# Kernel optimization log

Hardware: AMD Instinct MI355X
Metric: run time of the kernel (lower is better)

Reference implementation:

```python
import jax, jax.numpy as jnp
import numpy as np

EMBED_DIM = 1024
BATCH = 4
SEQ = 2048


def setup_inputs() -> dict:
    key = jax.random.key(0)
    ks = jax.random.split(key, 9)
    E = EMBED_DIM
    s = 1.0 / np.sqrt(E)
    inp = {
        "x": jax.random.normal(ks[0], (BATCH, SEQ, E), dtype=jnp.float32),
        "Wq": jax.random.uniform(ks[1], (E, E), jnp.float32, -s, s),
        "bq": jax.random.uniform(ks[2], (E,), jnp.float32, -s, s),
        "Wk": jax.random.uniform(ks[3], (E, E), jnp.float32, -s, s),
        "bk": jax.random.uniform(ks[4], (E,), jnp.float32, -s, s),
        "Wv": jax.random.uniform(ks[5], (E, E), jnp.float32, -s, s),
        "bv": jax.random.uniform(ks[6], (E,), jnp.float32, -s, s),
        "Wo": jax.random.uniform(ks[7], (E, E), jnp.float32, -s, s),
        "bo": jax.random.uniform(ks[8], (E,), jnp.float32, -s, s),
    }
    return inp


def reference(x, Wq, bq, Wk, bk, Wv, bv, Wo, bo):
    # x: [B, S, E]. Single-head attention over full embed_dim.
    scale = x.shape[-1] ** -0.5
    q = jnp.einsum("bse,ef->bsf", x, Wq.T) + bq
    k = jnp.einsum("bse,ef->bsf", x, Wk.T) + bk
    v = jnp.einsum("bse,ef->bsf", x, Wv.T) + bv
    scores = jnp.einsum("bqe,bke->bqk", q, k) * scale  # [B, S, S]
    attn = jax.nn.softmax(scores, axis=-1)             # dropout p=0 -> identity
    out = jnp.einsum("bqk,bke->bqe", attn, v)
    return jnp.einsum("bse,ef->bsf", out, Wo.T) + bo
```

## Files before the change

kernel.cpp:

```cpp
#include <hip/hip_runtime.h>
#include <hip/hip_bf16.h>


typedef __bf16 bf16_t;
typedef __bf16 bf16x8 __attribute__((ext_vector_type(8)));
typedef __bf16 bf16x4 __attribute__((ext_vector_type(4)));
typedef float  f32x16 __attribute__((ext_vector_type(16)));

__device__ __forceinline__ void async_copy16(const void* g, void* l) {
  __builtin_amdgcn_global_load_lds(
      (const __attribute__((address_space(1))) void*)g,
      (__attribute__((address_space(3))) void*)l, 16, 0, 0);
}

__device__ __forceinline__ void store_out(float* p, float v)  { *p = v; }
__device__ __forceinline__ void store_out(bf16_t* p, float v) { *p = (bf16_t)v; }

#define BM 128
#define BN 128
#define BKT 64

template <typename OutT, int NBIAS>
__global__ __launch_bounds__(256) void gemm_bt(
    const bf16_t* __restrict__ A, const bf16_t* __restrict__ B,
    OutT* __restrict__ C,
    const float* __restrict__ b0, const float* __restrict__ b1,
    const float* __restrict__ b2,
    int M, int N, int K, int lda, int ldb, int ldc, float scale,
    long long strideA, long long strideB, long long strideC) {
  const int z = blockIdx.z;
  A += (long long)z * strideA;
  B += (long long)z * strideB;
  C += (long long)z * strideC;

  int bx = blockIdx.x, by = blockIdx.y;
  {
    const int GX  = gridDim.x;
    const int id  = by * GX + bx;
    const int per = GX * 8;
    const int grp = id / per;
    const int rem = id - grp * per;
    by = grp * 8 + (rem & 7);
    bx = rem >> 3;
  }

  __shared__ __align__(16) bf16_t As[BM * BKT];
  __shared__ __align__(16) bf16_t Bs[BN * BKT];

  const int t    = threadIdx.x;
  const int lane = t & 63;
  const int w    = t >> 6;
  const int wm   = w & 1;
  const int wn   = w >> 1;
  const int tileM = by * BM;
  const int tileN = bx * BN;

  f32x16 acc[2][2] = {};

  for (int k0 = 0; k0 < K; k0 += BKT) {
#pragma unroll
    for (int i = 0; i < 4; ++i) {
      const int c   = t + 256 * i;
      const int row = c >> 3;
      const int cc  = c & 7;
      const int gcc = cc ^ (row & 7);
      const int ldsbase = ((t & ~63) + 256 * i) * 8;
      async_copy16(A + (long long)(tileM + row) * lda + k0 + gcc * 8, &As[ldsbase]);
      async_copy16(B + (long long)(tileN + row) * ldb + k0 + gcc * 8, &Bs[ldsbase]);
    }
    __syncthreads();

#pragma unroll
    for (int s = 0; s < 4; ++s) {
      const int kc = s + 4 * (lane >> 5);
      bf16x8 af[2], bfr[2];
#pragma unroll
      for (int ti = 0; ti < 2; ++ti) {
        const int row = wm * 64 + ti * 32 + (lane & 31);
        af[ti] = *(const bf16x8*)&As[row * BKT + ((kc ^ (row & 7)) * 8)];
      }
#pragma unroll
      for (int tj = 0; tj < 2; ++tj) {
        const int row = wn * 64 + tj * 32 + (lane & 31);
        bfr[tj] = *(const bf16x8*)&Bs[row * BKT + ((kc ^ (row & 7)) * 8)];
      }
#pragma unroll
      for (int ti = 0; ti < 2; ++ti)
#pragma unroll
        for (int tj = 0; tj < 2; ++tj)
          acc[ti][tj] = __builtin_amdgcn_mfma_f32_32x32x16_bf16(
              af[ti], bfr[tj], acc[ti][tj], 0, 0, 0);
    }
    __syncthreads();
  }

#pragma unroll
  for (int tj = 0; tj < 2; ++tj) {
    const int col = tileN + wn * 64 + tj * 32 + (lane & 31);
    float bv = 0.f;
    if (NBIAS == 1) bv = b0[col];
    if (NBIAS == 3) {
      const float* bp = col < 1024 ? b0 : (col < 2048 ? b1 : b2);
      bv = bp[col & 1023];
    }
#pragma unroll
    for (int ti = 0; ti < 2; ++ti) {
      const int rowb = tileM + wm * 64 + ti * 32 + 4 * (lane >> 5);
#pragma unroll
      for (int r = 0; r < 16; ++r) {
        const int row = rowb + (r & 3) + 8 * (r >> 2);
        store_out(&C[(long long)row * ldc + col], acc[ti][tj][r] * scale + bv);
      }
    }
  }
}

__global__ __launch_bounds__(256) void cast_all(
    const float4* __restrict__ w0, const float4* __restrict__ w1,
    const float4* __restrict__ w2, const float4* __restrict__ w3,
    const float4* __restrict__ x,
    bf16x4* __restrict__ wdst, bf16x4* __restrict__ xdst) {
  const int N4W = 1 << 18;
  const int id = blockIdx.x * 256 + threadIdx.x;
  const float4* src;
  bf16x4* dst;
  if (id < 4 * N4W) {
    const int z = id >> 18;
    src = (z == 0 ? w0 : z == 1 ? w1 : z == 2 ? w2 : w3) + (id & (N4W - 1));
    dst = wdst + id;
  } else {
    const int i = id - 4 * N4W;
    src = x + i;
    dst = xdst + i;
  }
  const float4 v = *src;
  bf16x4 o;
  o[0] = (bf16_t)v.x; o[1] = (bf16_t)v.y; o[2] = (bf16_t)v.z; o[3] = (bf16_t)v.w;
  *dst = o;
}

__global__ __launch_bounds__(256) void transpose_bf16(
    const bf16_t* __restrict__ in, bf16_t* __restrict__ out, int R, int C,
    int ldin, long long sIn, long long sOut) {
  in  += (long long)blockIdx.z * sIn;
  out += (long long)blockIdx.z * sOut;
  __shared__ bf16_t tile[32][33];
  const int tx = threadIdx.x, ty = threadIdx.y;
  const int x = blockIdx.x * 32 + tx;
  const int y0 = blockIdx.y * 32;
#pragma unroll
  for (int j = 0; j < 32; j += 8)
    tile[ty + j][tx] = in[(long long)(y0 + ty + j) * ldin + x];
  __syncthreads();
  const int x2 = y0 + tx;
  const int y2 = blockIdx.x * 32;
#pragma unroll
  for (int j = 0; j < 32; j += 8)
    out[(long long)(y2 + ty + j) * R + x2] = tile[tx][ty + j];
}

__global__ __launch_bounds__(256) void softmax_rows(
    const bf16_t* __restrict__ S, bf16_t* __restrict__ P, int cols) {
  const long long row = blockIdx.x;
  const bf16x8* inp = (const bf16x8*)(S + row * cols);
  bf16x8* outp      = (bf16x8*)(P + row * cols);
  const int t = threadIdx.x;
  const int w = t >> 6, lane = t & 63;

  const bf16x8 v = inp[t];
  float f[8];
#pragma unroll
  for (int j = 0; j < 8; ++j) f[j] = (float)v[j];

  float m = f[0];
#pragma unroll
  for (int j = 1; j < 8; ++j) m = fmaxf(m, f[j]);
#pragma unroll
  for (int off = 32; off > 0; off >>= 1) m = fmaxf(m, __shfl_xor(m, off));

  __shared__ float red[8];
  if (lane == 0) red[w] = m;
  __syncthreads();
  m = fmaxf(fmaxf(red[0], red[1]), fmaxf(red[2], red[3]));

  float e[8], sum = 0.f;
#pragma unroll
  for (int j = 0; j < 8; ++j) { e[j] = __expf(f[j] - m); sum += e[j]; }
#pragma unroll
  for (int off = 32; off > 0; off >>= 1) sum += __shfl_xor(sum, off);
  if (lane == 0) red[4 + w] = sum;
  __syncthreads();
  sum = red[4] + red[5] + red[6] + red[7];

  const float inv = 1.f / sum;
  bf16x8 o;
#pragma unroll
  for (int j = 0; j < 8; ++j) o[j] = (bf16_t)(e[j] * inv);
  outp[t] = o;
}

extern "C" void kernel_launch(void* const* d_in, const int* in_sizes, int n_in,
                              void* d_out, int out_size, void* d_ws, size_t ws_size,
                              hipStream_t stream) {
  const int E = 1024, S = 2048, B = 4;
  const int BS = B * S;

  const float* x  = (const float*)d_in[0];
  const float* Wq = (const float*)d_in[1];
  const float* bq = (const float*)d_in[2];
  const float* Wk = (const float*)d_in[3];
  const float* bk = (const float*)d_in[4];
  const float* Wv = (const float*)d_in[5];
  const float* bv = (const float*)d_in[6];
  const float* Wo = (const float*)d_in[7];
  const float* bo = (const float*)d_in[8];
  float* out = (float*)d_out;

  char* w = (char*)d_ws;
  const size_t MB = 1ull << 20;
  bf16_t* Wqkvb = (bf16_t*)(w + 0 * MB);
  bf16_t* Wob   = Wqkvb + 3 * E * E;
  bf16_t* xb    = (bf16_t*)(w + 8 * MB);
  bf16_t* QKVb  = (bf16_t*)(w + 24 * MB);
  bf16_t* VTb   = (bf16_t*)(w + 72 * MB);
  bf16_t* Sb    = (bf16_t*)(w + 88 * MB);
  bf16_t* Pb    = (bf16_t*)(w + 8 * MB);
  bf16_t* Ob    = (bf16_t*)(w + 40 * MB);

  {
    const int totalBlocks = ((4 << 18) + (1 << 21)) / 256;
    cast_all<<<totalBlocks, 256, 0, stream>>>(
        (const float4*)Wq, (const float4*)Wk, (const float4*)Wv,
        (const float4*)Wo, (const float4*)x, (bf16x4*)Wqkvb, (bf16x4*)xb);
  }

  gemm_bt<bf16_t, 3><<<dim3(3 * E / BN, BS / BM, 1), 256, 0, stream>>>(
      xb, Wqkvb, QKVb, bq, bk, bv,
      BS, 3 * E, E, E, E, 3 * E, 1.f, 0, 0, 0);

  transpose_bf16<<<dim3(E / 32, S / 32, B), dim3(32, 8), 0, stream>>>(
      QKVb + 2 * E, VTb, S, E, 3 * E, (long long)S * 3 * E, (long long)E * S);

  gemm_bt<bf16_t, 0><<<dim3(S / BN, S / BM, B), 256, 0, stream>>>(
      QKVb, QKVb + E, Sb, nullptr, nullptr, nullptr,
      S, S, E, 3 * E, 3 * E, S, 0.03125f,
      (long long)S * 3 * E, (long long)S * 3 * E, (long long)S * S);

  softmax_rows<<<BS, 256, 0, stream>>>(Sb, Pb, S);

  gemm_bt<bf16_t, 0><<<dim3(E / BN, S / BM, B), 256, 0, stream>>>(
      Pb, VTb, Ob, nullptr, nullptr, nullptr,
      S, E, S, S, S, E, 1.f,
      (long long)S * S, (long long)E * S, (long long)S * E);

  gemm_bt<float, 1><<<dim3(E / BN, BS / BM, 1), 256, 0, stream>>>(
      Ob, Wob, out, bo, nullptr, nullptr,
      BS, E, E, E, E, E, 1.f, 0, 0, 0);
}
```

Baseline: 292.2 us.

## Fuse softmax into score and PV GEMM epilogues, compute V transposed directly

```diff
diff --git a/kernel.cpp b/kernel.cpp
--- a/kernel.cpp
+++ b/kernel.cpp
@@ -20,18 +20,19 @@
 #define BN 128
 #define BKT 64
 
-template <typename OutT, int NBIAS>
+template <typename OutT, int BIAS, int EPI>
 __global__ __launch_bounds__(256) void gemm_bt(
     const bf16_t* __restrict__ A, const bf16_t* __restrict__ B,
     OutT* __restrict__ C,
     const float* __restrict__ b0, const float* __restrict__ b1,
-    const float* __restrict__ b2,
+    float* __restrict__ rsum, int rsStride,
     int M, int N, int K, int lda, int ldb, int ldc, float scale,
     long long strideA, long long strideB, long long strideC) {
   const int z = blockIdx.z;
   A += (long long)z * strideA;
   B += (long long)z * strideB;
   C += (long long)z * strideC;
+  if (EPI >= 1) rsum += (long long)z * rsStride;
 
   int bx = blockIdx.x, by = blockIdx.y;
   {
@@ -94,22 +95,50 @@
     __syncthreads();
   }
 
-#pragma unroll
-  for (int tj = 0; tj < 2; ++tj) {
-    const int col = tileN + wn * 64 + tj * 32 + (lane & 31);
-    float bv = 0.f;
-    if (NBIAS == 1) bv = b0[col];
-    if (NBIAS == 3) {
-      const float* bp = col < 1024 ? b0 : (col < 2048 ? b1 : b2);
-      bv = bp[col & 1023];
-    }
+  if (EPI == 0 && BIAS != 3) {
+#pragma unroll
+    for (int tj = 0; tj < 2; ++tj) {
+      const int col = tileN + wn * 64 + tj * 32 + (lane & 31);
+      float bv = 0.f;
+      if (BIAS == 1) bv = b0[col];
+      if (BIAS == 2) bv = (col < 1024 ? b0[col] : b1[col - 1024]);
+#pragma unroll
+      for (int ti = 0; ti < 2; ++ti) {
+        const int rowb = tileM + wm * 64 + ti * 32 + 4 * (lane >> 5);
+#pragma unroll
+        for (int r = 0; r < 16; ++r) {
+          const int row = rowb + (r & 3) + 8 * (r >> 2);
+          store_out(&C[(long long)row * ldc + col], acc[ti][tj][r] * scale + bv);
+        }
+      }
+    }
+  } else {
+    const int col0 = tileN + wn * 64 + (lane & 31);
 #pragma unroll
     for (int ti = 0; ti < 2; ++ti) {
       const int rowb = tileM + wm * 64 + ti * 32 + 4 * (lane >> 5);
 #pragma unroll
       for (int r = 0; r < 16; ++r) {
         const int row = rowb + (r & 3) + 8 * (r >> 2);
-        store_out(&C[(long long)row * ldc + col], acc[ti][tj][r] * scale + bv);
+        if (EPI == 1) {
+          const float e0 = __expf(acc[ti][0][r] * scale);
+          const float e1 = __expf(acc[ti][1][r] * scale);
+          store_out(&C[(long long)row * ldc + col0],      e0);
+          store_out(&C[(long long)row * ldc + col0 + 32], e1);
+          float s = e0 + e1;
+          s += __shfl_xor(s, 1);  s += __shfl_xor(s, 2);
+          s += __shfl_xor(s, 4);  s += __shfl_xor(s, 8);
+          s += __shfl_xor(s, 16);
+          if ((lane & 31) == 0) atomicAdd(&rsum[row], s);
+        } else if (EPI == 2) {
+          const float inv = 1.0f / rsum[row];
+          store_out(&C[(long long)row * ldc + col0],      acc[ti][0][r] * inv);
+          store_out(&C[(long long)row * ldc + col0 + 32], acc[ti][1][r] * inv);
+        } else {
+          const float bv = b0[row];
+          store_out(&C[(long long)row * ldc + col0],      acc[ti][0][r] * scale + bv);
+          store_out(&C[(long long)row * ldc + col0 + 32], acc[ti][1][r] * scale + bv);
+        }
       }
     }
   }
@@ -119,14 +148,21 @@
     const float4* __restrict__ w0, const float4* __restrict__ w1,
     const float4* __restrict__ w2, const float4* __restrict__ w3,
     const float4* __restrict__ x,
-    bf16x4* __restrict__ wdst, bf16x4* __restrict__ xdst) {
-  const int N4W = 1 << 18;
+    bf16x4* __restrict__ wdst, bf16x4* __restrict__ xdst,
+    float4* __restrict__ rsumv4) {
+  const int N4W  = 1 << 18;
+  const int BASE = 4 * N4W + (1 << 21);
   const int id = blockIdx.x * 256 + threadIdx.x;
+  if (id >= BASE) {
+    const int i = id - BASE;
+    if (i < 2048) rsumv4[i] = make_float4(0.f, 0.f, 0.f, 0.f);
+    return;
+  }
   const float4* src;
   bf16x4* dst;
   if (id < 4 * N4W) {
-    const int z = id >> 18;
-    src = (z == 0 ? w0 : z == 1 ? w1 : z == 2 ? w2 : w3) + (id & (N4W - 1));
+    const int zz = id >> 18;
+    src = (zz == 0 ? w0 : zz == 1 ? w1 : zz == 2 ? w2 : w3) + (id & (N4W - 1));
     dst = wdst + id;
   } else {
     const int i = id - 4 * N4W;
@@ -137,66 +173,6 @@
   bf16x4 o;
   o[0] = (bf16_t)v.x; o[1] = (bf16_t)v.y; o[2] = (bf16_t)v.z; o[3] = (bf16_t)v.w;
   *dst = o;
-}
-
-__global__ __launch_bounds__(256) void transpose_bf16(
-    const bf16_t* __restrict__ in, bf16_t* __restrict__ out, int R, int C,
-    int ldin, long long sIn, long long sOut) {
-  in  += (long long)blockIdx.z * sIn;
-  out += (long long)blockIdx.z * sOut;
-  __shared__ bf16_t tile[32][33];
-  const int tx = threadIdx.x, ty = threadIdx.y;
-  const int x = blockIdx.x * 32 + tx;
-  const int y0 = blockIdx.y * 32;
-#pragma unroll
-  for (int j = 0; j < 32; j += 8)
-    tile[ty + j][tx] = in[(long long)(y0 + ty + j) * ldin + x];
-  __syncthreads();
-  const int x2 = y0 + tx;
-  const int y2 = blockIdx.x * 32;
-#pragma unroll
-  for (int j = 0; j < 32; j += 8)
-    out[(long long)(y2 + ty + j) * R + x2] = tile[tx][ty + j];
-}
-
-__global__ __launch_bounds__(256) void softmax_rows(
-    const bf16_t* __restrict__ S, bf16_t* __restrict__ P, int cols) {
-  const long long row = blockIdx.x;
-  const bf16x8* inp = (const bf16x8*)(S + row * cols);
-  bf16x8* outp      = (bf16x8*)(P + row * cols);
-  const int t = threadIdx.x;
-  const int w = t >> 6, lane = t & 63;
-
-  const bf16x8 v = inp[t];
-  float f[8];
-#pragma unroll
-  for (int j = 0; j < 8; ++j) f[j] = (float)v[j];
-
-  float m = f[0];
-#pragma unroll
-  for (int j = 1; j < 8; ++j) m = fmaxf(m, f[j]);
-#pragma unroll
-  for (int off = 32; off > 0; off >>= 1) m = fmaxf(m, __shfl_xor(m, off));
-
-  __shared__ float red[8];
-  if (lane == 0) red[w] = m;
-  __syncthreads();
-  m = fmaxf(fmaxf(red[0], red[1]), fmaxf(red[2], red[3]));
-
-  float e[8], sum = 0.f;
-#pragma unroll
-  for (int j = 0; j < 8; ++j) { e[j] = __expf(f[j] - m); sum += e[j]; }
-#pragma unroll
-  for (int off = 32; off > 0; off >>= 1) sum += __shfl_xor(sum, off);
-  if (lane == 0) red[4 + w] = sum;
-  __syncthreads();
-  sum = red[4] + red[5] + red[6] + red[7];
-
-  const float inv = 1.f / sum;
-  bf16x8 o;
-#pragma unroll
-  for (int j = 0; j < 8; ++j) o[j] = (bf16_t)(e[j] * inv);
-  outp[t] = o;
 }
 
 extern "C" void kernel_launch(void* const* d_in, const int* in_sizes, int n_in,
@@ -219,41 +195,42 @@
   char* w = (char*)d_ws;
   const size_t MB = 1ull << 20;
   bf16_t* Wqkvb = (bf16_t*)(w + 0 * MB);
+  bf16_t* Wvb   = Wqkvb + 2 * E * E;
   bf16_t* Wob   = Wqkvb + 3 * E * E;
   bf16_t* xb    = (bf16_t*)(w + 8 * MB);
-  bf16_t* QKVb  = (bf16_t*)(w + 24 * MB);
-  bf16_t* VTb   = (bf16_t*)(w + 72 * MB);
-  bf16_t* Sb    = (bf16_t*)(w + 88 * MB);
-  bf16_t* Pb    = (bf16_t*)(w + 8 * MB);
-  bf16_t* Ob    = (bf16_t*)(w + 40 * MB);
+  bf16_t* Ob    = (bf16_t*)(w + 8 * MB);
+  bf16_t* QKb   = (bf16_t*)(w + 24 * MB);
+  bf16_t* VTb   = (bf16_t*)(w + 56 * MB);
+  bf16_t* Sb    = (bf16_t*)(w + 72 * MB);
+  float*  rsum  = (float*)(w + 104 * MB);
 
   {
-    const int totalBlocks = ((4 << 18) + (1 << 21)) / 256;
-    cast_all<<<totalBlocks, 256, 0, stream>>>(
+    const int blocks = ((4 << 18) + (1 << 21) + 2048) / 256;
+    cast_all<<<blocks, 256, 0, stream>>>(
         (const float4*)Wq, (const float4*)Wk, (const float4*)Wv,
-        (const float4*)Wo, (const float4*)x, (bf16x4*)Wqkvb, (bf16x4*)xb);
-  }
-
-  gemm_bt<bf16_t, 3><<<dim3(3 * E / BN, BS / BM, 1), 256, 0, stream>>>(
-      xb, Wqkvb, QKVb, bq, bk, bv,
-      BS, 3 * E, E, E, E, 3 * E, 1.f, 0, 0, 0);
-
-  transpose_bf16<<<dim3(E / 32, S / 32, B), dim3(32, 8), 0, stream>>>(
-      QKVb + 2 * E, VTb, S, E, 3 * E, (long long)S * 3 * E, (long long)E * S);
-
-  gemm_bt<bf16_t, 0><<<dim3(S / BN, S / BM, B), 256, 0, stream>>>(
-      QKVb, QKVb + E, Sb, nullptr, nullptr, nullptr,
-      S, S, E, 3 * E, 3 * E, S, 0.03125f,
-      (long long)S * 3 * E, (long long)S * 3 * E, (long long)S * S);
-
-  softmax_rows<<<BS, 256, 0, stream>>>(Sb, Pb, S);
-
-  gemm_bt<bf16_t, 0><<<dim3(E / BN, S / BM, B), 256, 0, stream>>>(
-      Pb, VTb, Ob, nullptr, nullptr, nullptr,
-      S, E, S, S, S, E, 1.f,
-      (long long)S * S, (long long)E * S, (long long)S * E);
-
-  gemm_bt<float, 1><<<dim3(E / BN, BS / BM, 1), 256, 0, stream>>>(
-      Ob, Wob, out, bo, nullptr, nullptr,
+        (const float4*)Wo, (const float4*)x,
+        (bf16x4*)Wqkvb, (bf16x4*)xb, (float4*)rsum);
+  }
+
+  gemm_bt<bf16_t, 2, 0><<<dim3(2 * E / BN, BS / BM, 1), 256, 0, stream>>>(
+      xb, Wqkvb, QKb, bq, bk, nullptr, 0,
+      BS, 2 * E, E, E, E, 2 * E, 1.f, 0, 0, 0);
+
+  gemm_bt<bf16_t, 3, 0><<<dim3(BS / BN, E / BM, 1), 256, 0, stream>>>(
+      Wvb, xb, VTb, bv, nullptr, nullptr, 0,
+      E, BS, E, E, E, BS, 1.f, 0, 0, 0);
+
+  gemm_bt<bf16_t, 0, 1><<<dim3(S / BN, S / BM, B), 256, 0, stream>>>(
+      QKb, QKb + E, Sb, nullptr, nullptr, rsum, S,
+      S, S, E, 2 * E, 2 * E, S, 0.03125f,
+      (long long)S * 2 * E, (long long)S * 2 * E, (long long)S * S);
+
+  gemm_bt<bf16_t, 0, 2><<<dim3(E / BN, S / BM, B), 256, 0, stream>>>(
+      Sb, VTb, Ob, nullptr, nullptr, rsum, S,
+      S, E, S, S, BS, E, 1.f,
+      (long long)S * S, (long long)S, (long long)S * E);
+
+  gemm_bt<float, 1, 0><<<dim3(E / BN, BS / BM, 1), 256, 0, stream>>>(
+      Ob, Wob, out, bo, nullptr, nullptr, 0,
       BS, E, E, E, E, E, 1.f, 0, 0, 0);
 }
```

Result: slower. 318.5 us (+9.0%).
